# Kernel tuning notes

Hardware: AMD Instinct MI355X
Metric: run time of the kernel (lower is better)

The kernel has to match this reference:

```python
import jax, jax.numpy as jnp
import numpy as np

BINS = 64
VMIN, VMAX = 0.0, 1.0


def _calc_histogram(x):
    # x: [B, C, H, W] float
    B, C, H, W = x.shape
    x_norm = jnp.clip((x - VMIN) / (VMAX - VMIN), 0.0, 1.0)
    flat = x_norm.reshape(B * C, H * W)
    # torch.histc semantics over [0,1]: bin i = [i/BINS, (i+1)/BINS), last bin closed.
    idx = jnp.clip((flat * BINS).astype(jnp.int32), 0, BINS - 1)  # [B*C, HW]
    row_offset = (jnp.arange(B * C, dtype=jnp.int32) * BINS)[:, None]
    flat_idx = (idx + row_offset).reshape(-1)
    counts = jax.ops.segment_sum(
        jnp.ones(flat_idx.shape, dtype=x.dtype), flat_idx,
        num_segments=B * C * BINS,
    ).reshape(B * C, BINS)
    counts = counts / jnp.clip(counts.sum(axis=1, keepdims=True), 1e-8, None)
    return counts.reshape(B, C, BINS)


def reference(fake_images, real_images):
    hist_fake = _calc_histogram(fake_images)
    hist_real = _calc_histogram(real_images)
    # loss_type == 'l1'
    return jnp.abs(hist_fake - hist_real).mean()


def setup_inputs() -> dict:
    key = jax.random.key(0)
    k1, k2 = jax.random.split(key)
    shape = (32, 3, 512, 512)
    fake_images = jax.random.uniform(k1, shape, dtype=jnp.float32)
    real_images = jax.random.uniform(k2, shape, dtype=jnp.float32)
    return {"fake_images": fake_images, "real_images": real_images}
```

## Files before the change

### kernel.cpp

```cpp
#include <hip/hip_runtime.h>
#include <hip/hip_bf16.h>


#define HW        262144
#define ROWS      96
#define NBINS     64
#define BPR       8
#define CHUNK     (HW / BPR)
#define THREADS   256
#define F4_ITERS  (CHUNK / 4 / THREADS)
#define NBLOCKS   (2 * ROWS * BPR)
#define PITCH_W   17

__global__ __launch_bounds__(THREADS)
void hist_kernel(const float* __restrict__ fake,
                 const float* __restrict__ real,
                 unsigned int* __restrict__ partial) {
    __shared__ unsigned int priv[THREADS * PITCH_W];
    __shared__ unsigned int comb[4][NBINS];

    const int tid  = threadIdx.x;
    const int lane = tid & 63;
    const int wv   = tid >> 6;

#pragma unroll
    for (int k = 0; k < PITCH_W; ++k) priv[tid * PITCH_W + k] = 0u;

    const int b     = blockIdx.x;
    const int chunk = b & (BPR - 1);
    const int rowg  = b >> 3;
    const float* src = (rowg < ROWS) ? fake : real;
    const int row    = (rowg < ROWS) ? rowg : (rowg - ROWS);

    const float4* __restrict__ p =
        (const float4*)(src + (size_t)row * HW + (size_t)chunk * CHUNK);

    unsigned char* my = (unsigned char*)&priv[tid * PITCH_W];

#pragma unroll 4
    for (int i = 0; i < F4_ITERS; ++i) {
        float4 v = p[i * THREADS + tid];
        int b0 = min((int)(v.x * 64.0f), 63);
        int b1 = min((int)(v.y * 64.0f), 63);
        int b2 = min((int)(v.z * 64.0f), 63);
        int b3 = min((int)(v.w * 64.0f), 63);
        my[b0]++;
        my[b1]++;
        my[b2]++;
        my[b3]++;
    }
    __syncthreads();

    const int cword = lane >> 2;
    const int shift = (lane & 3) * 8;
    unsigned cnt = 0;
#pragma unroll 8
    for (int t = 0; t < 64; ++t) {
        unsigned w32 = priv[(wv * 64 + t) * PITCH_W + cword];
        cnt += (w32 >> shift) & 0xffu;
    }
    comb[wv][lane] = cnt;
    __syncthreads();

    if (tid < NBINS) {
        unsigned s = comb[0][tid] + comb[1][tid] + comb[2][tid] + comb[3][tid];
        partial[(size_t)b * NBINS + tid] = s;
    }
}

__global__ __launch_bounds__(1024)
void loss_kernel(const unsigned int* __restrict__ partial,
                 float* __restrict__ out) {
    const int tid = threadIdx.x;
    int acc = 0;
#pragma unroll
    for (int q = 0; q < 6; ++q) {
        const int pIdx = q * 1024 + tid;
        const int r  = pIdx >> 6;
        const int bb = pIdx & 63;
        unsigned cf = 0, cr = 0;
#pragma unroll
        for (int c = 0; c < BPR; ++c) {
            cf += partial[((r * BPR + c) * NBINS) + bb];
            cr += partial[(((ROWS + r) * BPR + c) * NBINS) + bb];
        }
        int d = (int)cf - (int)cr;
        acc += (d < 0) ? -d : d;
    }
#pragma unroll
    for (int off = 32; off > 0; off >>= 1)
        acc += __shfl_down(acc, off, 64);
    __shared__ int wsum[16];
    if ((tid & 63) == 0) wsum[tid >> 6] = acc;
    __syncthreads();
    if (tid == 0) {
        long long total = 0;
#pragma unroll
        for (int k = 0; k < 16; ++k) total += wsum[k];
        out[0] = (float)((double)total / (262144.0 * 6144.0));
    }
}

extern "C" void kernel_launch(void* const* d_in, const int* in_sizes, int n_in,
                              void* d_out, int out_size, void* d_ws, size_t ws_size,
                              hipStream_t stream) {
    const float* fake = (const float*)d_in[0];
    const float* real = (const float*)d_in[1];
    unsigned int* partial = (unsigned int*)d_ws;
    float* out = (float*)d_out;

    hist_kernel<<<NBLOCKS, THREADS, 0, stream>>>(fake, real, partial);
    loss_kernel<<<1, 1024, 0, stream>>>(partial, out);
}
```

Before: 220.9 us.

## Replace LDS byte histogram with wave ballot bit-slicing and popcount counting

Drops the per-thread byte-packed shared-memory histogram and its reduction pass. For each element, the kernel now takes six wave-wide ballots of the bin-index bits. Each lane, which owns one bin, combines the masks with XOR/AND against its own lane bits and popcounts the matches into a register counter. This removes the LDS read-modify-write traffic and the LDS reduction, at the cost of about 30 VALU/SALU instructions per element in inline asm.

```diff
diff --git a/kernel.cpp b/kernel.cpp
--- a/kernel.cpp
+++ b/kernel.cpp
@@ -10,21 +10,71 @@
 #define THREADS   256
 #define F4_ITERS  (CHUNK / 4 / THREADS)
 #define NBLOCKS   (2 * ROWS * BPR)
-#define PITCH_W   17
+
+__device__ __forceinline__ void count_elem(float c,
+                                           unsigned x0, unsigned x1, unsigned x2,
+                                           unsigned x3, unsigned x4, unsigned x5,
+                                           unsigned& cnt) {
+    int bi = (int)(c * 64.0f);
+    bi = min(bi, 63);
+    unsigned long long m0 = __ballot(bi & 1);
+    unsigned long long m1 = __ballot(bi & 2);
+    unsigned long long m2 = __ballot(bi & 4);
+    unsigned long long m3 = __ballot(bi & 8);
+    unsigned long long m4 = __ballot(bi & 16);
+    unsigned long long m5 = __ballot(bi & 32);
+    unsigned a_lo, a_hi, t_lo, t_hi;
+    asm("v_xor_b32 %[alo], %[m0lo], %[x0]\n\t"
+        "v_xor_b32 %[ahi], %[m0hi], %[x0]\n\t"
+        "v_xor_b32 %[tlo], %[m1lo], %[x1]\n\t"
+        "v_xor_b32 %[thi], %[m1hi], %[x1]\n\t"
+        "v_and_b32 %[alo], %[alo], %[tlo]\n\t"
+        "v_and_b32 %[ahi], %[ahi], %[thi]\n\t"
+        "v_xor_b32 %[tlo], %[m2lo], %[x2]\n\t"
+        "v_xor_b32 %[thi], %[m2hi], %[x2]\n\t"
+        "v_and_b32 %[alo], %[alo], %[tlo]\n\t"
+        "v_and_b32 %[ahi], %[ahi], %[thi]\n\t"
+        "v_xor_b32 %[tlo], %[m3lo], %[x3]\n\t"
+        "v_xor_b32 %[thi], %[m3hi], %[x3]\n\t"
+        "v_and_b32 %[alo], %[alo], %[tlo]\n\t"
+        "v_and_b32 %[ahi], %[ahi], %[thi]\n\t"
+        "v_xor_b32 %[tlo], %[m4lo], %[x4]\n\t"
+        "v_xor_b32 %[thi], %[m4hi], %[x4]\n\t"
+        "v_and_b32 %[alo], %[alo], %[tlo]\n\t"
+        "v_and_b32 %[ahi], %[ahi], %[thi]\n\t"
+        "v_xor_b32 %[tlo], %[m5lo], %[x5]\n\t"
+        "v_xor_b32 %[thi], %[m5hi], %[x5]\n\t"
+        "v_and_b32 %[alo], %[alo], %[tlo]\n\t"
+        "v_and_b32 %[ahi], %[ahi], %[thi]\n\t"
+        "v_bcnt_u32_b32 %[cnt], %[alo], %[cnt]\n\t"
+        "v_bcnt_u32_b32 %[cnt], %[ahi], %[cnt]"
+        : [cnt] "+v"(cnt),
+          [alo] "=&v"(a_lo), [ahi] "=&v"(a_hi),
+          [tlo] "=&v"(t_lo), [thi] "=&v"(t_hi)
+        : [m0lo] "s"((unsigned)m0), [m0hi] "s"((unsigned)(m0 >> 32)),
+          [m1lo] "s"((unsigned)m1), [m1hi] "s"((unsigned)(m1 >> 32)),
+          [m2lo] "s"((unsigned)m2), [m2hi] "s"((unsigned)(m2 >> 32)),
+          [m3lo] "s"((unsigned)m3), [m3hi] "s"((unsigned)(m3 >> 32)),
+          [m4lo] "s"((unsigned)m4), [m4hi] "s"((unsigned)(m4 >> 32)),
+          [m5lo] "s"((unsigned)m5), [m5hi] "s"((unsigned)(m5 >> 32)),
+          [x0] "v"(x0), [x1] "v"(x1), [x2] "v"(x2),
+          [x3] "v"(x3), [x4] "v"(x4), [x5] "v"(x5));
+}
 
 __global__ __launch_bounds__(THREADS)
 void hist_kernel(const float* __restrict__ fake,
                  const float* __restrict__ real,
                  unsigned int* __restrict__ partial) {
-    __shared__ unsigned int priv[THREADS * PITCH_W];
-    __shared__ unsigned int comb[4][NBINS];
-
     const int tid  = threadIdx.x;
     const int lane = tid & 63;
     const int wv   = tid >> 6;
 
-#pragma unroll
-    for (int k = 0; k < PITCH_W; ++k) priv[tid * PITCH_W + k] = 0u;
+    const unsigned x0 = (lane & 1)  ? 0u : ~0u;
+    const unsigned x1 = (lane & 2)  ? 0u : ~0u;
+    const unsigned x2 = (lane & 4)  ? 0u : ~0u;
+    const unsigned x3 = (lane & 8)  ? 0u : ~0u;
+    const unsigned x4 = (lane & 16) ? 0u : ~0u;
+    const unsigned x5 = (lane & 32) ? 0u : ~0u;
 
     const int b     = blockIdx.x;
     const int chunk = b & (BPR - 1);
@@ -35,33 +85,20 @@
     const float4* __restrict__ p =
         (const float4*)(src + (size_t)row * HW + (size_t)chunk * CHUNK);
 
-    unsigned char* my = (unsigned char*)&priv[tid * PITCH_W];
+    unsigned cnt = 0;
 
 #pragma unroll 4
     for (int i = 0; i < F4_ITERS; ++i) {
         float4 v = p[i * THREADS + tid];
-        int b0 = min((int)(v.x * 64.0f), 63);
-        int b1 = min((int)(v.y * 64.0f), 63);
-        int b2 = min((int)(v.z * 64.0f), 63);
-        int b3 = min((int)(v.w * 64.0f), 63);
-        my[b0]++;
-        my[b1]++;
-        my[b2]++;
-        my[b3]++;
+        count_elem(v.x, x0, x1, x2, x3, x4, x5, cnt);
+        count_elem(v.y, x0, x1, x2, x3, x4, x5, cnt);
+        count_elem(v.z, x0, x1, x2, x3, x4, x5, cnt);
+        count_elem(v.w, x0, x1, x2, x3, x4, x5, cnt);
     }
-    __syncthreads();
 
-    const int cword = lane >> 2;
-    const int shift = (lane & 3) * 8;
-    unsigned cnt = 0;
-#pragma unroll 8
-    for (int t = 0; t < 64; ++t) {
-        unsigned w32 = priv[(wv * 64 + t) * PITCH_W + cword];
-        cnt += (w32 >> shift) & 0xffu;
-    }
+    __shared__ unsigned int comb[4][NBINS];
     comb[wv][lane] = cnt;
     __syncthreads();
-
     if (tid < NBINS) {
         unsigned s = comb[0][tid] + comb[1][tid] + comb[2][tid] + comb[3][tid];
         partial[(size_t)b * NBINS + tid] = s;
```

New measurement: 229.8 us. 4.0% more time.
